# Kernel tuning notes

Measured on AMD Instinct MI355X. Metric: run time of the kernel, lower is better.

## Reference

```python
import jax, jax.numpy as jnp
import numpy as np

N_NODES = 50000
N_EDGES = 600000
IN_F, HID_F, OUT_F = 128, 128, 64


def setup_inputs() -> dict:
    key = jax.random.key(0)
    ks = jax.random.split(key, 7)
    features = jax.random.normal(ks[0], (N_NODES, IN_F), jnp.float32)
    W1 = jax.random.normal(ks[1], (IN_F, HID_F), jnp.float32) / np.sqrt(IN_F)
    b1 = jnp.zeros((HID_F,), jnp.float32)
    W2 = jax.random.normal(ks[2], (HID_F, OUT_F), jnp.float32) / np.sqrt(HID_F)
    b2 = jnp.zeros((OUT_F,), jnp.float32)
    edge_src = jax.random.randint(ks[3], (N_EDGES,), 0, N_NODES, jnp.int32)
    edge_dst = jax.random.randint(ks[4], (N_EDGES,), 0, N_NODES, jnp.int32)
    return {"features": features, "W1": W1, "b1": b1, "W2": W2, "b2": b2,
            "edge_src": edge_src, "edge_dst": edge_dst}


def _graph_conv(h, W, b, edge_src, edge_dst, norm_src, norm_dst, n_nodes):
    # DGL GraphConv, norm='both': D_in^{-1/2} A D_out^{-1/2} (h W) + b
    # Apply W first (linear commutes with the linear aggregation) to minimize
    # the size of the gathered edge tensor when out <= in.
    h = (h * norm_src[:, None]) @ W                       # [N, d_out]
    agg = jax.ops.segment_sum(h[edge_src], edge_dst, num_segments=n_nodes)
    return agg * norm_dst[:, None] + b


def reference(features, W1, b1, W2, b2, edge_src, edge_dst):
    n_nodes = features.shape[0]
    ones = jnp.ones(edge_src.shape[0], features.dtype)
    out_deg = jax.ops.segment_sum(ones, edge_src, num_segments=n_nodes)
    in_deg = jax.ops.segment_sum(ones, edge_dst, num_segments=n_nodes)
    norm_src = jnp.clip(out_deg, 1.0) ** -0.5             # source-side D_out^{-1/2}
    norm_dst = jnp.clip(in_deg, 1.0) ** -0.5              # dest-side   D_in^{-1/2}
    h = _graph_conv(features, W1, b1, edge_src, edge_dst, norm_src, norm_dst, n_nodes)
    h = jax.nn.relu(h)
    h = _graph_conv(h, W2, b2, edge_src, edge_dst, norm_src, norm_dst, n_nodes)
    return h
```

## Files before the change

### kernel.cpp

```cpp
#include <hip/hip_runtime.h>


typedef unsigned short u16;
typedef unsigned int u32;
typedef short s16x8 __attribute__((ext_vector_type(8)));
typedef float f32x4 __attribute__((ext_vector_type(4)));
typedef u32 u32x4 __attribute__((ext_vector_type(4)));

__device__ __forceinline__ float bf2f(u16 u) {
    return __uint_as_float((u32)u << 16);
}
__device__ __forceinline__ u16 f2bf(float f) {
    u32 u = __float_as_uint(f);
    u += 0x7fff + ((u >> 16) & 1);
    return (u16)(u >> 16);
}


__global__ __launch_bounds__(256) void hist_part(const int* __restrict__ src,
                                                 const int* __restrict__ dst,
                                                 u32* __restrict__ part) {
    __shared__ u32 cnt[6250];
    const int s = blockIdx.x;
    const int r = blockIdx.y;
    const int z = blockIdx.z;
    const int lo = r * 12500;
    for (int t = threadIdx.x; t < 6250; t += 256) cnt[t] = 0;
    __syncthreads();
    const int* ids = z ? dst : src;
    const int base = s * 37500;
    for (int e0 = base; e0 < base + 37500; e0 += 1024) {
        int idx[4];
#pragma unroll
        for (int k = 0; k < 4; ++k) {
            int e = e0 + k * 256 + threadIdx.x;
            idx[k] = (e < base + 37500) ? ids[e] : -1;
        }
#pragma unroll
        for (int k = 0; k < 4; ++k) {
            unsigned local = (unsigned)(idx[k] - lo);
            if (local < 12500u)
                atomicAdd(&cnt[local >> 1], 1u << ((local & 1) * 16));
        }
    }
    __syncthreads();
    u32* out = part + (size_t)(z * 16 + s) * 25000 + r * 6250;
    for (int t = threadIdx.x; t < 6250; t += 256) out[t] = cnt[t];
}

__global__ __launch_bounds__(256) void reduce_norm_sniff(const u32* __restrict__ part,
                                                         int* __restrict__ degd,
                                                         float* __restrict__ ns,
                                                         float* __restrict__ nd,
                                                         int* __restrict__ bsum,
                                                         const u16* __restrict__ X16,
                                                         int* __restrict__ flag) {
    __shared__ int sh[256];
    if (blockIdx.x == 0) {
        u16 v = X16[threadIdx.x * 2];
        int e = (v >> 7) & 0xFF;
        sh[threadIdx.x] = (e >= 0x30 && e <= 0x47) ? 1 : 0;
        __syncthreads();
        for (int off = 128; off > 0; off >>= 1) {
            if (threadIdx.x < off) sh[threadIdx.x] += sh[threadIdx.x + off];
            __syncthreads();
        }
        if (threadIdx.x == 0) *flag = (sh[0] >= 128) ? 1 : 0;
        __syncthreads();
    }
    int i = blockIdx.x * 256 + threadIdx.x;
    u32 a = 0, b = 0;
    if (i < 50000) {
        const int w = i >> 1, h = (i & 1) * 16;
#pragma unroll
        for (int s = 0; s < 16; ++s) {
            a += (part[(size_t)s * 25000 + w] >> h) & 0xffffu;
            b += (part[(size_t)(16 + s) * 25000 + w] >> h) & 0xffffu;
        }
        degd[i] = (int)b;
        ns[i] = rsqrtf((float)(a > 1 ? a : 1));
        nd[i] = rsqrtf((float)(b > 1 ? b : 1));
    }
    sh[threadIdx.x] = (i < 50000) ? (int)b : 0;
    __syncthreads();
    for (int off = 128; off > 0; off >>= 1) {
        if (threadIdx.x < off) sh[threadIdx.x] += sh[threadIdx.x + off];
        __syncthreads();
    }
    if (threadIdx.x == 0) bsum[blockIdx.x] = sh[0];
}

__global__ __launch_bounds__(256) void rowptr_scan(const int* __restrict__ degd,
                                                   const int* __restrict__ bsum,
                                                   int* __restrict__ rp,
                                                   int* __restrict__ cur,
                                                   int n, int nb) {
    __shared__ int sb[256];
    __shared__ int sh[256];
    const int t = threadIdx.x;
    sb[t] = (t < nb && t < (int)blockIdx.x) ? bsum[t] : 0;
    int i = blockIdx.x * 256 + t;
    int v = (i < n) ? degd[i] : 0;
    sh[t] = v;
    __syncthreads();
    for (int off = 128; off > 0; off >>= 1) {
        if (t < off) sb[t] += sb[t + off];
        __syncthreads();
    }
    const int boff = sb[0];
    for (int off = 1; off < 256; off <<= 1) {
        int x = (t >= off) ? sh[t - off] : 0;
        __syncthreads();
        sh[t] += x;
        __syncthreads();
    }
    if (i < n) {
        int e = boff + sh[t] - v;
        rp[i] = e;
        cur[i] = e;
        if (i == n - 1) rp[n] = e + v;
    }
}

__global__ __launch_bounds__(256) void fill_kernel(const int* __restrict__ src,
                                                   const int* __restrict__ dst,
                                                   int* __restrict__ cur,
                                                   int* __restrict__ col, int n) {
    int i = blockIdx.x * 256 + threadIdx.x;
    if (i < n) {
        int pos = atomicAdd(&cur[dst[i]], 1);
        col[pos] = src[i];
    }
}

template <int FO, bool X_ALWAYS_BF16>
__global__ __launch_bounds__(256) void gemm_mfma(const void* __restrict__ Xv,
                                                 const void* __restrict__ Wv,
                                                 const int* __restrict__ flagp,
                                                 const float* __restrict__ ns,
                                                 u16* __restrict__ Ylo,
                                                 u16* __restrict__ Yhi,
                                                 int split, int nrows) {
    constexpr int NCT = FO / 64;
    __shared__ __align__(16) u32 Xs[64 * 68];
    const int flag = *flagp;
    const int tid = threadIdx.x;
    const int nb = blockIdx.x * 64;

    const bool xbf = X_ALWAYS_BF16 ? true : (flag != 0);
    if (xbf) {
        const u32* Xg = (const u32*)Xv;
        for (int t = tid; t < 64 * 64; t += 256) {
            int row = t >> 6, cp = t & 63;
            int r = nb + row;
            Xs[row * 68 + cp] = (r < nrows) ? Xg[(size_t)r * 64 + cp] : 0u;
        }
    } else {
        const float* Xg = (const float*)Xv;
        for (int t = tid; t < 64 * 64; t += 256) {
            int row = t >> 6, cp = t & 63;
            int r = nb + row;
            u32 lo = 0, hi = 0;
            if (r < nrows) {
                lo = f2bf(Xg[(size_t)r * 128 + 2 * cp]);
                hi = f2bf(Xg[(size_t)r * 128 + 2 * cp + 1]);
            }
            Xs[row * 68 + cp] = lo | (hi << 16);
        }
    }

    const int lane = tid & 63;
    const int wv = tid >> 6;
    const int lr = lane & 15;
    const int g = lane >> 4;
    const int cbase = wv * (FO / 4);

    u32 bf[NCT][4][4];
    if (flag) {
        const u32* Wg = (const u32*)Wv;
#pragma unroll
        for (int c = 0; c < NCT; ++c) {
            const int col = cbase + c * 16 + lr;
            const int ce = col >> 1, sh = (col & 1) * 16;
#pragma unroll
            for (int t = 0; t < 4; ++t)
#pragma unroll
                for (int p = 0; p < 4; ++p) {
                    const int kp = t * 16 + g * 4 + p;
                    u32 lo = (Wg[(size_t)(2 * kp) * (FO / 2) + ce] >> sh) & 0xffffu;
                    u32 hi = (Wg[(size_t)(2 * kp + 1) * (FO / 2) + ce] >> sh) & 0xffffu;
                    bf[c][t][p] = lo | (hi << 16);
                }
        }
    } else {
        const float* Wg = (const float*)Wv;
#pragma unroll
        for (int c = 0; c < NCT; ++c) {
            const int col = cbase + c * 16 + lr;
#pragma unroll
            for (int t = 0; t < 4; ++t)
#pragma unroll
                for (int p = 0; p < 4; ++p) {
                    const int kp = t * 16 + g * 4 + p;
                    u32 lo = f2bf(Wg[(size_t)(2 * kp) * FO + col]);
                    u32 hi = f2bf(Wg[(size_t)(2 * kp + 1) * FO + col]);
                    bf[c][t][p] = lo | (hi << 16);
                }
        }
    }
    __syncthreads();

    union U4 { u32x4 u; s16x8 s; };
#pragma unroll
    for (int rt = 0; rt < 4; ++rt) {
        U4 a[4];
#pragma unroll
        for (int t = 0; t < 4; ++t)
            a[t].u = *(const u32x4*)&Xs[(rt * 16 + lr) * 68 + t * 16 + g * 4];
        const int rq = nb + rt * 16 + g * 4;
        float nsv[4];
#pragma unroll
        for (int q = 0; q < 4; ++q) nsv[q] = ns[rq + q];
#pragma unroll
        for (int c = 0; c < NCT; ++c) {
            f32x4 acc = {0.f, 0.f, 0.f, 0.f};
#pragma unroll
            for (int t = 0; t < 4; ++t) {
                U4 b;
                b.u = (u32x4){bf[c][t][0], bf[c][t][1], bf[c][t][2], bf[c][t][3]};
                acc = __builtin_amdgcn_mfma_f32_16x16x32_bf16(a[t].s, b.s, acc,
                                                              0, 0, 0);
            }
            const int cc = cbase + c * 16 + lr;
#pragma unroll
            for (int q = 0; q < 4; ++q) {
                int r = rq + q;
                if (r < nrows) {
                    u16* Y = (r < split) ? (Ylo + (size_t)r * FO)
                                         : (Yhi + (size_t)(r - split) * FO);
                    Y[cc] = f2bf(acc[q] * nsv[q]);
                }
            }
        }
    }
}

__device__ __forceinline__ const u32* h128row(const u16* Hlo, const u16* Hhi,
                                              int split, int s) {
    return (const u32*)((s < split) ? (Hlo + (size_t)s * 128)
                                    : (Hhi + (size_t)(s - split) * 128));
}
__device__ __forceinline__ void g128_drain(const u16* __restrict__ Hlo,
                                           const u16* __restrict__ Hhi, int split,
                                           const int* __restrict__ col,
                                           int e, int pend, int lane,
                                           float& a0, float& a1) {
    for (; e + 8 <= pend; e += 8) {
        u32 u[8];
#pragma unroll
        for (int t = 0; t < 8; ++t)
            u[t] = h128row(Hlo, Hhi, split, col[e + t])[lane];
#pragma unroll
        for (int t = 0; t < 8; ++t) {
            a0 += bf2f((u16)(u[t] & 0xffff));
            a1 += bf2f((u16)(u[t] >> 16));
        }
    }
    for (; e + 4 <= pend; e += 4) {
        u32 u[4];
#pragma unroll
        for (int t = 0; t < 4; ++t)
            u[t] = h128row(Hlo, Hhi, split, col[e + t])[lane];
#pragma unroll
        for (int t = 0; t < 4; ++t) {
            a0 += bf2f((u16)(u[t] & 0xffff));
            a1 += bf2f((u16)(u[t] >> 16));
        }
    }
    for (; e < pend; ++e) {
        u32 u = h128row(Hlo, Hhi, split, col[e])[lane];
        a0 += bf2f((u16)(u & 0xffff));
        a1 += bf2f((u16)(u >> 16));
    }
}

__global__ __launch_bounds__(256) void gather128(const u16* __restrict__ Hlo,
                                                 const u16* __restrict__ Hhi, int split,
                                                 const int* __restrict__ rp,
                                                 const int* __restrict__ col,
                                                 const float* __restrict__ nd,
                                                 const void* __restrict__ bias,
                                                 const int* __restrict__ flagp,
                                                 u16* __restrict__ out, int nnodes) {
    int wv = threadIdx.x >> 6, lane = threadIdx.x & 63;
    int n0 = blockIdx.x * 8 + wv * 2;
    if (n0 >= nnodes) return;
    int n1 = n0 + 1;
    int pa = rp[n0], pae = rp[n0 + 1];
    int pb = rp[n1], pbe = rp[n1 + 1];
    float a0 = 0.f, a1 = 0.f, b0 = 0.f, b1 = 0.f;
    while (pa + 8 <= pae && pb + 8 <= pbe) {
        int sa[8], sb[8];
#pragma unroll
        for (int t = 0; t < 8; ++t) sa[t] = col[pa + t];
#pragma unroll
        for (int t = 0; t < 8; ++t) sb[t] = col[pb + t];
        u32 ua[8], ub[8];
#pragma unroll
        for (int t = 0; t < 8; ++t) ua[t] = h128row(Hlo, Hhi, split, sa[t])[lane];
#pragma unroll
        for (int t = 0; t < 8; ++t) ub[t] = h128row(Hlo, Hhi, split, sb[t])[lane];
#pragma unroll
        for (int t = 0; t < 8; ++t) {
            a0 += bf2f((u16)(ua[t] & 0xffff));
            a1 += bf2f((u16)(ua[t] >> 16));
            b0 += bf2f((u16)(ub[t] & 0xffff));
            b1 += bf2f((u16)(ub[t] >> 16));
        }
        pa += 8;
        pb += 8;
    }
    g128_drain(Hlo, Hhi, split, col, pa, pae, lane, a0, a1);
    g128_drain(Hlo, Hhi, split, col, pb, pbe, lane, b0, b1);
    int flag = *flagp;
    float bb0 = flag ? bf2f(((const u16*)bias)[lane * 2]) : ((const float*)bias)[lane * 2];
    float bb1 = flag ? bf2f(((const u16*)bias)[lane * 2 + 1]) : ((const float*)bias)[lane * 2 + 1];
    float va = nd[n0], vb = nd[n1];
    u32 pa32 = (u32)f2bf(fmaxf(a0 * va + bb0, 0.f))
             | ((u32)f2bf(fmaxf(a1 * va + bb1, 0.f)) << 16);
    u32 pb32 = (u32)f2bf(fmaxf(b0 * vb + bb0, 0.f))
             | ((u32)f2bf(fmaxf(b1 * vb + bb1, 0.f)) << 16);
    ((u32*)(out + (size_t)n0 * 128))[lane] = pa32;
    ((u32*)(out + (size_t)n1 * 128))[lane] = pb32;
}

__device__ __forceinline__ void g64_drain(const u16* __restrict__ H,
                                          const int* __restrict__ col,
                                          int e, int pend, int lane, float& a) {
    for (; e + 8 <= pend; e += 8) {
        float f[8];
#pragma unroll
        for (int t = 0; t < 8; ++t)
            f[t] = bf2f(H[(size_t)col[e + t] * 64 + lane]);
#pragma unroll
        for (int t = 0; t < 8; ++t) a += f[t];
    }
    for (; e + 4 <= pend; e += 4) {
        float f[4];
#pragma unroll
        for (int t = 0; t < 4; ++t)
            f[t] = bf2f(H[(size_t)col[e + t] * 64 + lane]);
#pragma unroll
        for (int t = 0; t < 4; ++t) a += f[t];
    }
    for (; e < pend; ++e)
        a += bf2f(H[(size_t)col[e] * 64 + lane]);
}

__global__ __launch_bounds__(256) void gather64(const u16* __restrict__ H,
                                                const int* __restrict__ rp,
                                                const int* __restrict__ col,
                                                const float* __restrict__ nd,
                                                const void* __restrict__ bias,
                                                const int* __restrict__ flagp,
                                                void* __restrict__ outv, int nnodes) {
    int wv = threadIdx.x >> 6, lane = threadIdx.x & 63;
    int n0 = blockIdx.x * 8 + wv * 2;
    if (n0 >= nnodes) return;
    int n1 = n0 + 1;
    int pa = rp[n0], pae = rp[n0 + 1];
    int pb = rp[n1], pbe = rp[n1 + 1];
    float a = 0.f, b = 0.f;
    while (pa + 8 <= pae && pb + 8 <= pbe) {
        float fa[8], fb[8];
#pragma unroll
        for (int t = 0; t < 8; ++t)
            fa[t] = bf2f(H[(size_t)col[pa + t] * 64 + lane]);
#pragma unroll
        for (int t = 0; t < 8; ++t)
            fb[t] = bf2f(H[(size_t)col[pb + t] * 64 + lane]);
#pragma unroll
        for (int t = 0; t < 8; ++t) { a += fa[t]; b += fb[t]; }
        pa += 8;
        pb += 8;
    }
    g64_drain(H, col, pa, pae, lane, a);
    g64_drain(H, col, pb, pbe, lane, b);
    int flag = *flagp;
    float bb = flag ? bf2f(((const u16*)bias)[lane]) : ((const float*)bias)[lane];
    float oa = a * nd[n0] + bb;
    float ob = b * nd[n1] + bb;
    if (flag) {
        ((u16*)outv)[(size_t)n0 * 64 + lane] = f2bf(oa);
        ((u16*)outv)[(size_t)n1 * 64 + lane] = f2bf(ob);
    } else {
        ((float*)outv)[(size_t)n0 * 64 + lane] = oa;
        ((float*)outv)[(size_t)n1 * 64 + lane] = ob;
    }
}

extern "C" void kernel_launch(void* const* d_in, const int* in_sizes, int n_in,
                              void* d_out, int out_size, void* d_ws, size_t ws_size,
                              hipStream_t stream) {
    constexpr int N = 50000;
    constexpr int E = 600000;
    constexpr int NB = (N + 255) / 256;
    constexpr int SPLIT = 25000;

    const void* X  = d_in[0];
    const void* W1 = d_in[1];
    const void* b1 = d_in[2];
    const void* W2 = d_in[3];
    const void* b2 = d_in[4];
    const int* esrc = (const int*)d_in[5];
    const int* edst = (const int*)d_in[6];

    char* p = (char*)d_ws;
    auto take = [&](size_t bytes) -> char* {
        char* r = p;
        p += (bytes + 255) & ~(size_t)255;
        return r;
    };
    int* flagp  = (int*)take(256);
    int* deg_d  = (int*)take((size_t)N * 4);
    float* ns   = (float*)take((size_t)N * 4);
    float* nd   = (float*)take((size_t)N * 4);
    int* bsum   = (int*)take((size_t)NB * 4);
    int* rp     = (int*)take((size_t)(N + 1) * 4);
    int* cur    = (int*)take((size_t)N * 4);
    int* col    = (int*)take((size_t)E * 4);
    u16* h0hi   = (u16*)take((size_t)(N - SPLIT) * 128 * 2);
    u16* a2     = (u16*)take((size_t)N * 128 * 2);
    size_t NEED = (size_t)(p - (char*)d_ws);

    if (ws_size < NEED) {
        hipMemsetAsync(d_out, 0, (size_t)out_size * 2, stream);
        return;
    }

    u16* h0lo = (u16*)d_out;

    u32* part = (u32*)a2;

    hist_part<<<dim3(16, 4, 2), 256, 0, stream>>>(esrc, edst, part);
    reduce_norm_sniff<<<NB, 256, 0, stream>>>(part, deg_d, ns, nd, bsum,
                                              (const u16*)X, flagp);
    rowptr_scan<<<NB, 256, 0, stream>>>(deg_d, bsum, rp, cur, N, NB);
    fill_kernel<<<(E + 255) / 256, 256, 0, stream>>>(esrc, edst, cur, col, E);

    gemm_mfma<128, false><<<(N + 63) / 64, 256, 0, stream>>>(
        X, W1, flagp, ns, h0lo, h0hi, SPLIT, N);
    gather128<<<(N + 7) / 8, 256, 0, stream>>>(h0lo, h0hi, SPLIT, rp, col, nd,
                                               b1, flagp, a2, N);

    u16* h1b = h0hi;
    gemm_mfma<64, true><<<(N + 63) / 64, 256, 0, stream>>>(
        a2, W2, flagp, ns, h1b, h1b, N, N);
    gather64<<<(N + 7) / 8, 256, 0, stream>>>(h1b, rp, col, nd, b2, flagp,
                                              d_out, N);

    (void)in_sizes; (void)n_in; (void)out_size;
}
```

Measured before the change: 224.1 us.

## Fuse layer-1 gather with layer-2 GEMM through shared memory

```diff
diff --git a/kernel.cpp b/kernel.cpp
--- a/kernel.cpp
+++ b/kernel.cpp
@@ -284,54 +284,128 @@
     }
 }
 
-__global__ __launch_bounds__(256) void gather128(const u16* __restrict__ Hlo,
-                                                 const u16* __restrict__ Hhi, int split,
-                                                 const int* __restrict__ rp,
-                                                 const int* __restrict__ col,
-                                                 const float* __restrict__ nd,
-                                                 const void* __restrict__ bias,
-                                                 const int* __restrict__ flagp,
-                                                 u16* __restrict__ out, int nnodes) {
-    int wv = threadIdx.x >> 6, lane = threadIdx.x & 63;
-    int n0 = blockIdx.x * 8 + wv * 2;
-    if (n0 >= nnodes) return;
-    int n1 = n0 + 1;
-    int pa = rp[n0], pae = rp[n0 + 1];
-    int pb = rp[n1], pbe = rp[n1 + 1];
-    float a0 = 0.f, a1 = 0.f, b0 = 0.f, b1 = 0.f;
-    while (pa + 8 <= pae && pb + 8 <= pbe) {
-        int sa[8], sb[8];
-#pragma unroll
-        for (int t = 0; t < 8; ++t) sa[t] = col[pa + t];
-#pragma unroll
-        for (int t = 0; t < 8; ++t) sb[t] = col[pb + t];
-        u32 ua[8], ub[8];
-#pragma unroll
-        for (int t = 0; t < 8; ++t) ua[t] = h128row(Hlo, Hhi, split, sa[t])[lane];
-#pragma unroll
-        for (int t = 0; t < 8; ++t) ub[t] = h128row(Hlo, Hhi, split, sb[t])[lane];
-#pragma unroll
-        for (int t = 0; t < 8; ++t) {
-            a0 += bf2f((u16)(ua[t] & 0xffff));
-            a1 += bf2f((u16)(ua[t] >> 16));
-            b0 += bf2f((u16)(ub[t] & 0xffff));
-            b1 += bf2f((u16)(ub[t] >> 16));
-        }
-        pa += 8;
-        pb += 8;
-    }
-    g128_drain(Hlo, Hhi, split, col, pa, pae, lane, a0, a1);
-    g128_drain(Hlo, Hhi, split, col, pb, pbe, lane, b0, b1);
-    int flag = *flagp;
-    float bb0 = flag ? bf2f(((const u16*)bias)[lane * 2]) : ((const float*)bias)[lane * 2];
-    float bb1 = flag ? bf2f(((const u16*)bias)[lane * 2 + 1]) : ((const float*)bias)[lane * 2 + 1];
-    float va = nd[n0], vb = nd[n1];
-    u32 pa32 = (u32)f2bf(fmaxf(a0 * va + bb0, 0.f))
-             | ((u32)f2bf(fmaxf(a1 * va + bb1, 0.f)) << 16);
-    u32 pb32 = (u32)f2bf(fmaxf(b0 * vb + bb0, 0.f))
-             | ((u32)f2bf(fmaxf(b1 * vb + bb1, 0.f)) << 16);
-    ((u32*)(out + (size_t)n0 * 128))[lane] = pa32;
-    ((u32*)(out + (size_t)n1 * 128))[lane] = pb32;
+__global__ __launch_bounds__(512) void gather_gemm2(
+        const u16* __restrict__ Hlo, const u16* __restrict__ Hhi, int split,
+        const int* __restrict__ rp, const int* __restrict__ col,
+        const float* __restrict__ nd, const void* __restrict__ bias,
+        const void* __restrict__ Wv, const int* __restrict__ flagp,
+        const float* __restrict__ ns, u16* __restrict__ Y, int nnodes) {
+    __shared__ __align__(16) u32 Xs[64 * 68];
+    const int flag = *flagp;
+    const int tid = threadIdx.x;
+    const int lane = tid & 63;
+    const int wv = tid >> 6;
+    const int nb = blockIdx.x * 64;
+    const int lr = lane & 15;
+    const int g = lane >> 4;
+    const int cw = wv & 3, rh = wv >> 2;
+    const int cbase = cw * 16;
+
+    u32 bfr[4][4];
+    if (flag) {
+        const u32* Wg = (const u32*)Wv;
+        const int colc = cbase + lr;
+        const int ce = colc >> 1, sh = (colc & 1) * 16;
+#pragma unroll
+        for (int t = 0; t < 4; ++t)
+#pragma unroll
+            for (int p = 0; p < 4; ++p) {
+                const int kp = t * 16 + g * 4 + p;
+                u32 lo = (Wg[(size_t)(2 * kp) * 32 + ce] >> sh) & 0xffffu;
+                u32 hi = (Wg[(size_t)(2 * kp + 1) * 32 + ce] >> sh) & 0xffffu;
+                bfr[t][p] = lo | (hi << 16);
+            }
+    } else {
+        const float* Wg = (const float*)Wv;
+        const int colc = cbase + lr;
+#pragma unroll
+        for (int t = 0; t < 4; ++t)
+#pragma unroll
+            for (int p = 0; p < 4; ++p) {
+                const int kp = t * 16 + g * 4 + p;
+                u32 lo = f2bf(Wg[(size_t)(2 * kp) * 64 + colc]);
+                u32 hi = f2bf(Wg[(size_t)(2 * kp + 1) * 64 + colc]);
+                bfr[t][p] = lo | (hi << 16);
+            }
+    }
+
+    float bb0 = flag ? bf2f(((const u16*)bias)[lane * 2])
+                     : ((const float*)bias)[lane * 2];
+    float bb1 = flag ? bf2f(((const u16*)bias)[lane * 2 + 1])
+                     : ((const float*)bias)[lane * 2 + 1];
+
+    for (int j = 0; j < 4; ++j) {
+        const int row0 = wv * 8 + 2 * j;
+        const int n0 = nb + row0, n1 = n0 + 1;
+        if (n0 >= nnodes) {
+            Xs[row0 * 68 + lane] = 0u;
+            Xs[(row0 + 1) * 68 + lane] = 0u;
+            continue;
+        }
+        int pa = rp[n0], pae = rp[n0 + 1];
+        int pb = rp[n1], pbe = rp[n1 + 1];
+        float a0 = 0.f, a1 = 0.f, b0 = 0.f, b1 = 0.f;
+        while (pa + 8 <= pae && pb + 8 <= pbe) {
+            int sa[8], sb[8];
+#pragma unroll
+            for (int t = 0; t < 8; ++t) sa[t] = col[pa + t];
+#pragma unroll
+            for (int t = 0; t < 8; ++t) sb[t] = col[pb + t];
+            u32 ua[8], ub[8];
+#pragma unroll
+            for (int t = 0; t < 8; ++t) ua[t] = h128row(Hlo, Hhi, split, sa[t])[lane];
+#pragma unroll
+            for (int t = 0; t < 8; ++t) ub[t] = h128row(Hlo, Hhi, split, sb[t])[lane];
+#pragma unroll
+            for (int t = 0; t < 8; ++t) {
+                a0 += bf2f((u16)(ua[t] & 0xffff));
+                a1 += bf2f((u16)(ua[t] >> 16));
+                b0 += bf2f((u16)(ub[t] & 0xffff));
+                b1 += bf2f((u16)(ub[t] >> 16));
+            }
+            pa += 8;
+            pb += 8;
+        }
+        g128_drain(Hlo, Hhi, split, col, pa, pae, lane, a0, a1);
+        g128_drain(Hlo, Hhi, split, col, pb, pbe, lane, b0, b1);
+        const float va = nd[n0], vb = nd[n1];
+        Xs[row0 * 68 + lane] =
+            (u32)f2bf(fmaxf(a0 * va + bb0, 0.f))
+            | ((u32)f2bf(fmaxf(a1 * va + bb1, 0.f)) << 16);
+        Xs[(row0 + 1) * 68 + lane] =
+            (u32)f2bf(fmaxf(b0 * vb + bb0, 0.f))
+            | ((u32)f2bf(fmaxf(b1 * vb + bb1, 0.f)) << 16);
+    }
+    __syncthreads();
+
+    union U4 { u32x4 u; s16x8 s; };
+#pragma unroll
+    for (int rr = 0; rr < 2; ++rr) {
+        const int rt = rh * 2 + rr;
+        U4 a[4];
+#pragma unroll
+        for (int t = 0; t < 4; ++t)
+            a[t].u = *(const u32x4*)&Xs[(rt * 16 + lr) * 68 + t * 16 + g * 4];
+        const int rq = nb + rt * 16 + g * 4;
+        float nsv[4];
+#pragma unroll
+        for (int q = 0; q < 4; ++q) nsv[q] = ns[rq + q];
+        f32x4 acc = {0.f, 0.f, 0.f, 0.f};
+#pragma unroll
+        for (int t = 0; t < 4; ++t) {
+            U4 b;
+            b.u = (u32x4){bfr[t][0], bfr[t][1], bfr[t][2], bfr[t][3]};
+            acc = __builtin_amdgcn_mfma_f32_16x16x32_bf16(a[t].s, b.s, acc,
+                                                          0, 0, 0);
+        }
+        const int cc = cbase + lr;
+#pragma unroll
+        for (int q = 0; q < 4; ++q) {
+            int r = rq + q;
+            if (r < nnodes)
+                Y[(size_t)r * 64 + cc] = f2bf(acc[q] * nsv[q]);
+        }
+    }
 }
 
 __device__ __forceinline__ void g64_drain(const u16* __restrict__ H,
@@ -441,6 +515,7 @@
     u16* h0lo = (u16*)d_out;
 
     u32* part = (u32*)a2;
+    u16* h1b = a2;
 
     hist_part<<<dim3(16, 4, 2), 256, 0, stream>>>(esrc, edst, part);
     reduce_norm_sniff<<<NB, 256, 0, stream>>>(part, deg_d, ns, nd, bsum,
@@ -450,12 +525,8 @@
 
     gemm_mfma<128, false><<<(N + 63) / 64, 256, 0, stream>>>(
         X, W1, flagp, ns, h0lo, h0hi, SPLIT, N);
-    gather128<<<(N + 7) / 8, 256, 0, stream>>>(h0lo, h0hi, SPLIT, rp, col, nd,
-                                               b1, flagp, a2, N);
-
-    u16* h1b = h0hi;
-    gemm_mfma<64, true><<<(N + 63) / 64, 256, 0, stream>>>(
-        a2, W2, flagp, ns, h1b, h1b, N, N);
+    gather_gemm2<<<(N + 63) / 64, 512, 0, stream>>>(
+        h0lo, h0hi, SPLIT, rp, col, nd, b1, W2, flagp, ns, h1b, N);
     gather64<<<(N + 7) / 8, 256, 0, stream>>>(h1b, rp, col, nd, b2, flagp,
                                               d_out, N);
 
```

Result: slower. 233.0 us (+4.0%).
